# Kernel optimization log

Hardware: AMD Instinct MI355X
Metric: run time of the kernel (lower is better)

The kernel has to match this reference:

```python
import jax, jax.numpy as jnp
import numpy as np

M, K, L, OUT = 16, 64, 6, 128
IN_CH = 2 + 1 + 1 + 1 + 4 * L  # 29
HID_IN = 128 * 2 + 4           # 260


def setup_inputs() -> dict:
    key = jax.random.key(0)
    ks = jax.random.split(key, 5)
    N = 2_000_000
    P = jax.random.normal(ks[0], (N, 2), jnp.float32) * 2.0
    def lin(k, i, o):
        return jax.random.normal(k, (i, o), jnp.float32) / np.float32(np.sqrt(i))
    return {
        'P': P,
        'W1': lin(ks[1], IN_CH, 64), 'b1': jnp.zeros((64,), jnp.float32),
        'W2': lin(ks[2], 64, 128),   'b2': jnp.zeros((128,), jnp.float32),
        'W3': lin(ks[3], HID_IN, 128), 'b3': jnp.zeros((128,), jnp.float32),
        'W4': lin(ks[4], 128, OUT),  'b4': jnp.zeros((OUT,), jnp.float32),
    }


def _fps(P, m):
    # furthest point sampling, seeded at index 0 (standard convention)
    N = P.shape[0]
    def step(carry, _):
        min_d, last_idx = carry
        last = P[last_idx]
        d = jnp.sum((P - last) ** 2, axis=-1)          # [N]
        min_d = jnp.minimum(min_d, d)
        nxt = jnp.argmax(min_d)
        return (min_d, nxt), last_idx
    init = (jnp.full((N,), jnp.finfo(jnp.float32).max, jnp.float32), jnp.int32(0))
    (_, _), idxs = jax.lax.scan(step, init, None, length=m)
    return idxs  # [m] int


def _gelu(x):
    return jax.nn.gelu(x, approximate=False)  # torch nn.GELU default = erf


def reference(P, W1, b1, W2, b2, W3, b3, W4, b4):
    c_idx = jax.lax.stop_gradient(_fps(P, M))
    C = P[c_idx]                                       # [M,2]
    # brute-force kNN: expanded squared distance avoids [M,N,2] intermediate
    Ps = jax.lax.stop_gradient(P)
    Cs = jax.lax.stop_gradient(C)
    d2 = (jnp.sum(Ps ** 2, -1)[None, :]
          - 2.0 * Cs @ Ps.T
          + jnp.sum(Cs ** 2, -1)[:, None])             # [M,N]
    _, nidx = jax.lax.top_k(-d2, K)                    # [M,K]
    patch = P[nidx]                                    # [M,K,2]
    delta = patch - C[:, None, :]                      # [M,K,2]
    r = jnp.linalg.norm(delta, axis=-1, keepdims=True) # [M,K,1]
    theta = jnp.arctan2(delta[..., 1:2], delta[..., 0:1])
    freqs = (2.0 ** jnp.arange(L)).astype(jnp.float32) # [L]
    ang = delta[..., None, :] * freqs[:, None]         # [M,K,L,2]
    ff = jnp.concatenate([jnp.sin(ang), jnp.cos(ang)], -1).reshape(M, K, 4 * L)
    per_pt = jnp.concatenate([delta, r, jnp.sin(theta), jnp.cos(theta), ff], -1)  # [M,K,29]
    h = _gelu(per_pt @ W1 + b1)
    h = _gelu(h @ W2 + b2)                             # [M,K,128]
    h_max = h.max(axis=1)
    h_mean = h.mean(axis=1)
    rr = r[..., 0]                                     # [M,K]
    stats = jnp.stack([rr.mean(1), rr.max(1), rr.min(1), rr.std(1, ddof=1)], -1)  # [M,4]
    z = jnp.concatenate([h_max, h_mean, stats], -1)    # [M,260]
    F = _gelu(z @ W3 + b3) @ W4 + b4                   # [M,OUT]
    return F, C
```

## Files before the change

kernel.cpp:

```cpp
#include <hip/hip_runtime.h>
#include <math.h>

#define MCENT 16
#define KNN   64
#define NBINS 512
#define RBINS 256
#define CAP   7936
#define SKEYS 1024
#define FPSB  1024
#define FPST  256
#define MLPT  1024

__device__ __forceinline__ float gelu_f(float x){
    return 0.5f * x * (1.0f + erff(x * 0.70710678118654752440f));
}

__device__ __forceinline__ void xcd_slice(int NP, int B, int bid, int tpb, int tid,
                                          int* q0, int* s1, int* step){
    int xcd = bid & 7, j = bid >> 3, Bx = B >> 3;
    long long np = NP;
    *q0   = (int)((np * xcd) >> 3) + j*tpb + tid;
    *s1   = (int)((np * (xcd+1)) >> 3);
    *step = Bx * tpb;
}

__global__ __launch_bounds__(FPST) void fps_step(
    const float* __restrict__ P, int N,
    float* __restrict__ min_d,
    unsigned long long* __restrict__ partials,
    int k,
    float* __restrict__ cxy,
    float* __restrict__ outC,
    unsigned int* __restrict__ ghist,
    unsigned int* __restrict__ cnt)
{
    const int lane = threadIdx.x & 63;
    const int wid  = threadIdx.x >> 6;
    __shared__ unsigned long long wred[FPST/64];
    __shared__ int s_cur;

    if (k == 0){
        int gi = blockIdx.x*FPST + threadIdx.x;
        if (gi < MCENT*NBINS) ghist[gi] = 0u;
        if (gi < MCENT) cnt[gi] = 0u;
    }

    int cur = 0;
    if (k > 0){
        unsigned long long pb = 0ULL;
        for (int i = threadIdx.x; i < FPSB; i += FPST){
            unsigned long long v = partials[(k-1)*FPSB + i];
            if (v > pb) pb = v;
        }
#pragma unroll
        for (int off = 32; off > 0; off >>= 1){
            unsigned long long o = __shfl_xor(pb, off, 64);
            if (o > pb) pb = o;
        }
        if (lane == 0) wred[wid] = pb;
        __syncthreads();
        if (threadIdx.x == 0){
            unsigned long long b = wred[0];
#pragma unroll
            for (int w = 1; w < FPST/64; ++w) if (wred[w] > b) b = wred[w];
            s_cur = (int)(0xFFFFFFFFu - (unsigned)(b & 0xFFFFFFFFu));
        }
        __syncthreads();
        cur = s_cur;
    }

    if (blockIdx.x == 0 && threadIdx.x == 0){
        float cx = P[2*cur], cy = P[2*cur+1];
        cxy[2*k] = cx; cxy[2*k+1] = cy;
        outC[2*k] = cx; outC[2*k+1] = cy;
    }

    const float cx = P[2*cur], cy = P[2*cur+1];
    unsigned long long bk = 0ULL;
    const int NP = N >> 1;
    int q0, s1, st;
    xcd_slice(NP, gridDim.x, blockIdx.x, FPST, threadIdx.x, &q0, &s1, &st);
    for (int q = q0; q < s1; q += st){
        float4 p = ((const float4*)P)[q];
        float dx0 = __fsub_rn(p.x, cx), dy0 = __fsub_rn(p.y, cy);
        float d0  = __fadd_rn(__fmul_rn(dx0,dx0), __fmul_rn(dy0,dy0));
        float dx1 = __fsub_rn(p.z, cx), dy1 = __fsub_rn(p.w, cy);
        float d1  = __fadd_rn(__fmul_rn(dx1,dx1), __fmul_rn(dy1,dy1));
        float mx, my;
        if (k == 0){
            mx = d0; my = d1;
            ((float2*)min_d)[q] = make_float2(mx, my);
        } else {
            float2 mo = ((const float2*)min_d)[q];
            mx = fminf(mo.x, d0); my = fminf(mo.y, d1);
            if (mx != mo.x || my != mo.y)
                ((float2*)min_d)[q] = make_float2(mx, my);
        }
        int g = 2*q;
        unsigned long long k0 =
            ((unsigned long long)__float_as_uint(mx) << 32)
            | (unsigned long long)(0xFFFFFFFFu - (unsigned)g);
        unsigned long long k1 =
            ((unsigned long long)__float_as_uint(my) << 32)
            | (unsigned long long)(0xFFFFFFFFu - (unsigned)(g+1));
        if (k0 > bk) bk = k0;
        if (k1 > bk) bk = k1;
    }
    if ((N & 1) && blockIdx.x == 0 && threadIdx.x == 0){
        int g = N-1;
        float dx = __fsub_rn(P[2*g], cx), dy = __fsub_rn(P[2*g+1], cy);
        float d  = __fadd_rn(__fmul_rn(dx,dx), __fmul_rn(dy,dy));
        float nm = (k == 0) ? d : fminf(min_d[g], d);
        min_d[g] = nm;
        unsigned long long kk =
            ((unsigned long long)__float_as_uint(nm) << 32)
            | (unsigned long long)(0xFFFFFFFFu - (unsigned)g);
        if (kk > bk) bk = kk;
    }
#pragma unroll
    for (int off = 32; off > 0; off >>= 1){
        unsigned long long o = __shfl_xor(bk, off, 64);
        if (o > bk) bk = o;
    }
    if (lane == 0) wred[wid] = bk;
    __syncthreads();
    if (threadIdx.x == 0){
        unsigned long long b = wred[0];
#pragma unroll
        for (int w = 1; w < FPST/64; ++w) if (wred[w] > b) b = wred[w];
        partials[k*FPSB + blockIdx.x] = b;
    }
}

__global__ __launch_bounds__(256) void hist_kernel(
    const float* __restrict__ P, int N,
    const unsigned long long* __restrict__ partials,
    float* __restrict__ cxy,
    float* __restrict__ outC,
    unsigned int* __restrict__ ghist,
    unsigned int* __restrict__ rhist)
{
    __shared__ unsigned int h[MCENT*NBINS];
    __shared__ float scx[MCENT], scy[MCENT], scs2[MCENT];
    __shared__ unsigned long long wred[4];
    __shared__ int s_cur;

    {
        unsigned long long pb = 0ULL;
        for (int i = threadIdx.x; i < FPSB; i += 256){
            unsigned long long v = partials[14*FPSB + i];
            if (v > pb) pb = v;
        }
#pragma unroll
        for (int off = 32; off > 0; off >>= 1){
            unsigned long long o = __shfl_xor(pb, off, 64);
            if (o > pb) pb = o;
        }
        if ((threadIdx.x & 63) == 0) wred[threadIdx.x >> 6] = pb;
        __syncthreads();
        if (threadIdx.x == 0){
            unsigned long long b = wred[0];
#pragma unroll
            for (int w = 1; w < 4; ++w) if (wred[w] > b) b = wred[w];
            s_cur = (int)(0xFFFFFFFFu - (unsigned)(b & 0xFFFFFFFFu));
        }
        __syncthreads();
    }
    const int cur15 = s_cur;
    const float c15x = P[2*cur15], c15y = P[2*cur15+1];
    if (blockIdx.x == 0 && threadIdx.x == 0){
        cxy[30] = c15x; cxy[31] = c15y;
        outC[30] = c15x; outC[31] = c15y;
    }

    {
        int gi = blockIdx.x*blockDim.x + threadIdx.x;
        if (gi < MCENT*RBINS) rhist[gi] = 0u;
    }
    for (int i = threadIdx.x; i < MCENT*NBINS; i += blockDim.x) h[i] = 0u;
    if (threadIdx.x < MCENT){
        float a, b;
        if (threadIdx.x == 15){ a = c15x; b = c15y; }
        else { a = cxy[2*threadIdx.x]; b = cxy[2*threadIdx.x+1]; }
        scx[threadIdx.x] = a; scy[threadIdx.x] = b;
        scs2[threadIdx.x] = __fadd_rn(__fmul_rn(a,a), __fmul_rn(b,b));
    }
    __syncthreads();
    const int T    = gridDim.x * blockDim.x;
    const int NP16 = (N >> 1) >> 4;
    for (int q = blockIdx.x*blockDim.x + threadIdx.x; q < NP16; q += T){
        float4 p = ((const float4*)P)[(size_t)q << 4];
        float ps20 = __fadd_rn(__fmul_rn(p.x,p.x), __fmul_rn(p.y,p.y));
        float ps21 = __fadd_rn(__fmul_rn(p.z,p.z), __fmul_rn(p.w,p.w));
#pragma unroll
        for (int m = 0; m < MCENT; ++m){
            float dot0 = __fadd_rn(__fmul_rn(scx[m],p.x), __fmul_rn(scy[m],p.y));
            float d20  = __fadd_rn(__fsub_rn(ps20, __fmul_rn(2.0f,dot0)), scs2[m]);
            atomicAdd(&h[m*NBINS + (__float_as_uint(fmaxf(d20,0.0f)) >> 22)], 1u);
            float dot1 = __fadd_rn(__fmul_rn(scx[m],p.z), __fmul_rn(scy[m],p.w));
            float d21  = __fadd_rn(__fsub_rn(ps21, __fmul_rn(2.0f,dot1)), scs2[m]);
            atomicAdd(&h[m*NBINS + (__float_as_uint(fmaxf(d21,0.0f)) >> 22)], 1u);
        }
    }
    __syncthreads();
    for (int i = threadIdx.x; i < MCENT*NBINS; i += blockDim.x){
        unsigned v = h[i];
        if (v) atomicAdd(&ghist[i], v);
    }
}

__device__ __forceinline__ void compute_ssc(const unsigned* gh, int tid, float* ssc){
    if (tid < MCENT){
        unsigned cum = 0; int B = NBINS-1;
        for (int b = 0; b < NBINS; ++b){
            cum += gh[tid*NBINS + b];
            if (cum >= KNN){ B = b; break; }
        }
        ssc[tid] = 255.0f / __uint_as_float((unsigned)(B+1) << 22);
    }
}

__global__ __launch_bounds__(256) void refine_kernel(
    const float* __restrict__ P, int N,
    const float* __restrict__ cxy,
    const unsigned int* __restrict__ ghist,
    unsigned int* __restrict__ rhist)
{
    __shared__ unsigned int gh[MCENT*NBINS];
    __shared__ unsigned int h[MCENT*RBINS];
    __shared__ float scx[MCENT], scy[MCENT], scs2[MCENT], ssc[MCENT];
    for (int i = threadIdx.x; i < MCENT*NBINS; i += 256) gh[i] = ghist[i];
    for (int i = threadIdx.x; i < MCENT*RBINS; i += 256) h[i] = 0u;
    if (threadIdx.x < MCENT){
        float a = cxy[2*threadIdx.x], b = cxy[2*threadIdx.x+1];
        scx[threadIdx.x]=a; scy[threadIdx.x]=b;
        scs2[threadIdx.x]=__fadd_rn(__fmul_rn(a,a),__fmul_rn(b,b));
    }
    __syncthreads();
    compute_ssc(gh, threadIdx.x, ssc);
    __syncthreads();
    const int NP = N >> 1;
    int q0, s1, st;
    xcd_slice(NP, gridDim.x, blockIdx.x, 256, threadIdx.x, &q0, &s1, &st);
    for (int q = q0; q < s1; q += st){
        float4 p = ((const float4*)P)[q];
        float ps20 = __fadd_rn(__fmul_rn(p.x,p.x), __fmul_rn(p.y,p.y));
        float ps21 = __fadd_rn(__fmul_rn(p.z,p.z), __fmul_rn(p.w,p.w));
#pragma unroll
        for (int m = 0; m < MCENT; ++m){
            float dot0 = __fadd_rn(__fmul_rn(scx[m],p.x), __fmul_rn(scy[m],p.y));
            float d20  = __fadd_rn(__fsub_rn(ps20, __fmul_rn(2.0f,dot0)), scs2[m]);
            int b0 = (int)(fmaxf(d20, 0.0f) * ssc[m]);
            if (b0 < RBINS) atomicAdd(&h[m*RBINS + b0], 1u);
            float dot1 = __fadd_rn(__fmul_rn(scx[m],p.z), __fmul_rn(scy[m],p.w));
            float d21  = __fadd_rn(__fsub_rn(ps21, __fmul_rn(2.0f,dot1)), scs2[m]);
            int b1 = (int)(fmaxf(d21, 0.0f) * ssc[m]);
            if (b1 < RBINS) atomicAdd(&h[m*RBINS + b1], 1u);
        }
    }
    if ((N & 1) && blockIdx.x == 0 && threadIdx.x == 0){
        int g = N-1;
        float x = P[2*g], y = P[2*g+1];
        float ps2 = __fadd_rn(__fmul_rn(x,x), __fmul_rn(y,y));
        for (int m = 0; m < MCENT; ++m){
            float dot = __fadd_rn(__fmul_rn(scx[m],x), __fmul_rn(scy[m],y));
            float d2  = __fadd_rn(__fsub_rn(ps2, __fmul_rn(2.0f,dot)), scs2[m]);
            int b = (int)(fmaxf(d2, 0.0f) * ssc[m]);
            if (b < RBINS) atomicAdd(&h[m*RBINS + b], 1u);
        }
    }
    __syncthreads();
    for (int i = threadIdx.x; i < MCENT*RBINS; i += blockDim.x){
        unsigned v = h[i];
        if (v) atomicAdd(&rhist[i], v);
    }
}

__global__ __launch_bounds__(256) void collect_kernel(
    const float* __restrict__ P, int N,
    const float* __restrict__ cxy,
    const unsigned int* __restrict__ ghist,
    const unsigned int* __restrict__ rhist,
    unsigned int* __restrict__ cnt,
    float* __restrict__ cd2,
    int* __restrict__ cidx)
{
    __shared__ unsigned int gh[MCENT*NBINS];
    __shared__ unsigned int rh[MCENT*RBINS];
    __shared__ float scx[MCENT], scy[MCENT], scs2[MCENT], ssc[MCENT];
    __shared__ int sB2[MCENT];
    for (int i = threadIdx.x; i < MCENT*NBINS; i += 256) gh[i] = ghist[i];
    for (int i = threadIdx.x; i < MCENT*RBINS; i += 256) rh[i] = rhist[i];
    if (threadIdx.x < MCENT){
        float a = cxy[2*threadIdx.x], b = cxy[2*threadIdx.x+1];
        scx[threadIdx.x]=a; scy[threadIdx.x]=b;
        scs2[threadIdx.x]=__fadd_rn(__fmul_rn(a,a),__fmul_rn(b,b));
    }
    __syncthreads();
    compute_ssc(gh, threadIdx.x, ssc);
    if (threadIdx.x < MCENT){
        unsigned cum = 0; int B = RBINS-1;
        for (int b = 0; b < RBINS; ++b){
            cum += rh[threadIdx.x*RBINS + b];
            if (cum >= KNN){ B = b; break; }
        }
        sB2[threadIdx.x] = B;
    }
    __syncthreads();
    const int NP = N >> 1;
    int q0, s1, st;
    xcd_slice(NP, gridDim.x, blockIdx.x, 256, threadIdx.x, &q0, &s1, &st);
    for (int q = q0; q < s1; q += st){
        float4 p = ((const float4*)P)[q];
        float ps20 = __fadd_rn(__fmul_rn(p.x,p.x), __fmul_rn(p.y,p.y));
        float ps21 = __fadd_rn(__fmul_rn(p.z,p.z), __fmul_rn(p.w,p.w));
        int g = 2*q;
#pragma unroll
        for (int m = 0; m < MCENT; ++m){
            float dot0 = __fadd_rn(__fmul_rn(scx[m],p.x), __fmul_rn(scy[m],p.y));
            float d20  = __fadd_rn(__fsub_rn(ps20, __fmul_rn(2.0f,dot0)), scs2[m]);
            if ((int)(fmaxf(d20,0.0f) * ssc[m]) <= sB2[m]){
                unsigned pos = atomicAdd(&cnt[m], 1u);
                if (pos < CAP){ cd2[m*CAP+pos]=d20; cidx[m*CAP+pos]=g; }
            }
            float dot1 = __fadd_rn(__fmul_rn(scx[m],p.z), __fmul_rn(scy[m],p.w));
            float d21  = __fadd_rn(__fsub_rn(ps21, __fmul_rn(2.0f,dot1)), scs2[m]);
            if ((int)(fmaxf(d21,0.0f) * ssc[m]) <= sB2[m]){
                unsigned pos = atomicAdd(&cnt[m], 1u);
                if (pos < CAP){ cd2[m*CAP+pos]=d21; cidx[m*CAP+pos]=g+1; }
            }
        }
    }
    if ((N & 1) && blockIdx.x == 0 && threadIdx.x == 0){
        int g = N-1;
        float x = P[2*g], y = P[2*g+1];
        float ps2 = __fadd_rn(__fmul_rn(x,x), __fmul_rn(y,y));
        for (int m = 0; m < MCENT; ++m){
            float dot = __fadd_rn(__fmul_rn(scx[m],x), __fmul_rn(scy[m],y));
            float d2  = __fadd_rn(__fsub_rn(ps2, __fmul_rn(2.0f,dot)), scs2[m]);
            if ((int)(fmaxf(d2,0.0f) * ssc[m]) <= sB2[m]){
                unsigned pos = atomicAdd(&cnt[m], 1u);
                if (pos < CAP){ cd2[m*CAP+pos]=d2; cidx[m*CAP+pos]=g; }
            }
        }
    }
}

__global__ __launch_bounds__(MLPT) void mlp_kernel(
    const float* __restrict__ P,
    const float* __restrict__ cxy,
    const unsigned int* __restrict__ cnt,
    const float* __restrict__ cd2,
    const int* __restrict__ cidx,
    const float* __restrict__ W1, const float* __restrict__ b1,
    const float* __restrict__ W2, const float* __restrict__ b2,
    const float* __restrict__ W3, const float* __restrict__ b3,
    const float* __restrict__ W4, const float* __restrict__ b4,
    float* __restrict__ outF)
{
    const int m = blockIdx.x;
    const int tid = threadIdx.x;
    __shared__ float feat[KNN][32];
    __shared__ float h1s[KNN][64];
    __shared__ float sW1[29*64];
    __shared__ float sW2[64*128];
    __shared__ float pmax[8][128], psum[8][128];
    __shared__ float z[260];
    __shared__ float part[8][128];
    __shared__ float zz[128];
    __shared__ unsigned long long kkeys[SKEYS];
    __shared__ int snbr[KNN];

    {
        const float4* s2 = (const float4*)W2;
        float4* d2 = (float4*)sW2;
        d2[tid]        = s2[tid];
        d2[tid + 1024] = s2[tid + 1024];
        if (tid < 464) ((float4*)sW1)[tid] = ((const float4*)W1)[tid];
    }

    unsigned c = cnt[m]; if (c > CAP) c = CAP;
    if (c <= SKEYS){
        if (tid < (int)c){
            unsigned u = __float_as_uint(cd2[m*CAP+tid]);
            u = (u & 0x80000000u) ? ~u : (u | 0x80000000u);
            kkeys[tid] = ((unsigned long long)u << 32)
                       | (unsigned long long)(unsigned)cidx[m*CAP+tid];
        }
        __syncthreads();
        if (tid < (int)c){
            unsigned long long ki = kkeys[tid];
            int rank = 0;
            for (int j = 0; j < (int)c; ++j) rank += (kkeys[j] < ki);
            if (rank < KNN) snbr[rank] = (int)(unsigned)(ki & 0xFFFFFFFFu);
        }
    } else {
        for (int i = tid; i < (int)c; i += MLPT){
            unsigned ui = __float_as_uint(cd2[m*CAP+i]);
            ui = (ui & 0x80000000u) ? ~ui : (ui | 0x80000000u);
            unsigned long long ki = ((unsigned long long)ui << 32)
                                  | (unsigned long long)(unsigned)cidx[m*CAP+i];
            int rank = 0;
            for (int j = 0; j < (int)c; ++j){
                unsigned uj = __float_as_uint(cd2[m*CAP+j]);
                uj = (uj & 0x80000000u) ? ~uj : (uj | 0x80000000u);
                unsigned long long kj = ((unsigned long long)uj << 32)
                                      | (unsigned long long)(unsigned)cidx[m*CAP+j];
                rank += (kj < ki);
            }
            if (rank < KNN) snbr[rank] = (int)(unsigned)(ki & 0xFFFFFFFFu);
        }
    }
    __syncthreads();

    const float cx = cxy[2*m], cy = cxy[2*m+1];
    if (tid < KNN){
        int g = snbr[tid];
        float dx = P[2*g]   - cx;
        float dy = P[2*g+1] - cy;
        float r  = sqrtf(dx*dx + dy*dy);
        float th = atan2f(dy, dx);
        feat[tid][0]=dx; feat[tid][1]=dy; feat[tid][2]=r;
        feat[tid][3]=sinf(th); feat[tid][4]=cosf(th);
        float fx = dx, fy = dy;
#pragma unroll
        for (int l = 0; l < 6; ++l){
            feat[tid][5+4*l+0]=sinf(fx);
            feat[tid][5+4*l+1]=sinf(fy);
            feat[tid][5+4*l+2]=cosf(fx);
            feat[tid][5+4*l+3]=cosf(fy);
            fx += fx; fy += fy;
        }
    }
    __syncthreads();

#pragma unroll
    for (int rep = 0; rep < 4; ++rep){
        int o = rep*MLPT + tid;
        int k = o >> 6, j = o & 63;
        float acc = b1[j];
#pragma unroll
        for (int cc = 0; cc < 29; ++cc) acc += feat[k][cc] * sW1[cc*64 + j];
        h1s[k][j] = gelu_f(acc);
    }
    __syncthreads();

    {
        int j = tid & 127, kh = tid >> 7;
        float lmax = -3.402823466e+38f, lsum = 0.f;
        for (int kk = 0; kk < 8; ++kk){
            int k = kh*8 + kk;
            float acc = b2[j];
#pragma unroll 8
            for (int i = 0; i < 64; ++i) acc += h1s[k][i] * sW2[i*128 + j];
            float v = gelu_f(acc);
            lmax = fmaxf(lmax, v);
            lsum += v;
        }
        pmax[kh][j] = lmax; psum[kh][j] = lsum;
    }
    __syncthreads();
    if (tid < 128){
        float mx = pmax[0][tid], sm = psum[0][tid];
#pragma unroll
        for (int w = 1; w < 8; ++w){ mx = fmaxf(mx, pmax[w][tid]); sm += psum[w][tid]; }
        z[tid]       = mx;
        z[128 + tid] = sm * (1.0f/64.0f);
    }
    if (tid >= 128 && tid < 192){
        int l = tid - 128;
        float r = feat[l][2];
        float s = r, mx = r, mn = r;
        for (int off = 1; off < 64; off <<= 1){
            s  += __shfl_xor(s, off, 64);
            mx  = fmaxf(mx, __shfl_xor(mx, off, 64));
            mn  = fminf(mn, __shfl_xor(mn, off, 64));
        }
        float mean = s * (1.0f/64.0f);
        float dv = (r-mean)*(r-mean);
        for (int off = 1; off < 64; off <<= 1) dv += __shfl_xor(dv, off, 64);
        if (l == 0){
            z[256]=mean; z[257]=mx; z[258]=mn; z[259]=sqrtf(dv*(1.0f/63.0f));
        }
    }
    __syncthreads();

    {
        int j = tid & 127, seg = tid >> 7;
        int i0  = (seg < 4) ? seg*33 : 132 + (seg-4)*32;
        int cntn = (seg < 4) ? 33 : 32;
        float acc = 0.f;
        for (int i = i0; i < i0 + cntn; ++i) acc += z[i]*W3[i*128+j];
        part[seg][j] = acc;
    }
    __syncthreads();
    if (tid < 128){
        float a = part[0][tid];
#pragma unroll
        for (int w = 1; w < 8; ++w) a += part[w][tid];
        zz[tid] = gelu_f(a + b3[tid]);
    }
    __syncthreads();
    {
        int j = tid & 127, seg = tid >> 7;
        float acc = 0.f;
#pragma unroll
        for (int i = seg*16; i < seg*16+16; ++i) acc += zz[i]*W4[i*128+j];
        part[seg][j] = acc;
    }
    __syncthreads();
    if (tid < 128){
        float a = part[0][tid];
#pragma unroll
        for (int w = 1; w < 8; ++w) a += part[w][tid];
        outF[m*128 + tid] = a + b4[tid];
    }
}

extern "C" void kernel_launch(void* const* d_in, const int* in_sizes, int n_in,
                              void* d_out, int out_size, void* d_ws, size_t ws_size,
                              hipStream_t stream)
{
    const float* P  = (const float*)d_in[0];
    const float* W1 = (const float*)d_in[1];
    const float* b1 = (const float*)d_in[2];
    const float* W2 = (const float*)d_in[3];
    const float* b2 = (const float*)d_in[4];
    const float* W3 = (const float*)d_in[5];
    const float* b3 = (const float*)d_in[6];
    const float* W4 = (const float*)d_in[7];
    const float* b4 = (const float*)d_in[8];
    int N = in_sizes[0] / 2;
    float* outF = (float*)d_out;
    float* outC = outF + MCENT*128;
    (void)n_in; (void)out_size; (void)ws_size;

    char* base = (char*)d_ws;
    size_t off = 0;
    auto take = [&](size_t bytes)->char*{
        char* p = base + off;
        off = (off + bytes + 255) & ~(size_t)255;
        return p;
    };
    unsigned long long* partials = (unsigned long long*)take((size_t)MCENT*FPSB*8);
    float* cxy         = (float*)take(MCENT*2*4);
    unsigned int* ghist= (unsigned int*)take(MCENT*NBINS*4);
    unsigned int* rhist= (unsigned int*)take(MCENT*RBINS*4);
    unsigned int* cnt  = (unsigned int*)take(MCENT*4);
    float* cd2         = (float*)take((size_t)MCENT*CAP*4);
    int*   cidx        = (int*)  take((size_t)MCENT*CAP*4);
    float* min_d       = (float*)take((size_t)N*4);

    for (int k = 0; k < MCENT-1; ++k)
        fps_step<<<FPSB, FPST, 0, stream>>>(P, N, min_d, partials, k, cxy, outC,
                                            ghist, cnt);

    hist_kernel<<<128, 256, 0, stream>>>(P, N, partials, cxy, outC, ghist, rhist);
    refine_kernel<<<256, 256, 0, stream>>>(P, N, cxy, ghist, rhist);
    collect_kernel<<<512, 256, 0, stream>>>(P, N, cxy, ghist, rhist, cnt, cd2, cidx);
    mlp_kernel<<<MCENT, MLPT, 0, stream>>>(P, cxy, cnt, cd2, cidx,
                                           W1,b1,W2,b2,W3,b3,W4,b4, outF);
}
```

Before: 308.2 us.

## Fuse FPS iterations into one persistent cooperative kernel with register-resident points

Replaces the 15 per-iteration FPS kernel launches with a single cooperative kernel of 512x256 threads. Each thread keeps 16 points and their running min-distance in registers, and blocks synchronise across the grid through spin-waited atomic partials. This removes the per-step reloads of P and min_d from global memory and the launch overhead. The per-block histogram-threshold scans are moved into tiny separate kernels, and refine/collect now launch more blocks. The costs are spin-wait synchronisation, reliance on co-residency of all 512 blocks (enforced by the launch bounds of 2 blocks per CU), and extra small launches.

```diff
diff --git a/kernel.cpp b/kernel.cpp
--- a/kernel.cpp
+++ b/kernel.cpp
@@ -7,8 +7,9 @@
 #define RBINS 256
 #define CAP   7936
 #define SKEYS 1024
-#define FPSB  1024
+#define FPSB  512
 #define FPST  256
+#define NPT   16
 #define MLPT  1024
 
 __device__ __forceinline__ float gelu_f(float x){
@@ -24,32 +25,90 @@
     *step = Bx * tpb;
 }
 
-__global__ __launch_bounds__(FPST) void fps_step(
+__global__ void init_kernel(unsigned int* __restrict__ ghist,
+                            unsigned int* __restrict__ cnt,
+                            unsigned long long* __restrict__ partials){
+    const int T = gridDim.x * blockDim.x;
+    int t = blockIdx.x * blockDim.x + threadIdx.x;
+    for (int i = t; i < MCENT*NBINS; i += T) ghist[i] = 0u;
+    for (int i = t; i < (MCENT-1)*FPSB; i += T) partials[i] = 0ULL;
+    if (t < MCENT) cnt[t] = 0u;
+}
+
+__global__ __launch_bounds__(FPST, 2) void fps_coop(
     const float* __restrict__ P, int N,
-    float* __restrict__ min_d,
     unsigned long long* __restrict__ partials,
-    int k,
     float* __restrict__ cxy,
-    float* __restrict__ outC,
-    unsigned int* __restrict__ ghist,
-    unsigned int* __restrict__ cnt)
+    float* __restrict__ outC)
 {
+    const int T = FPSB * FPST;
+    const int t = blockIdx.x * FPST + threadIdx.x;
     const int lane = threadIdx.x & 63;
     const int wid  = threadIdx.x >> 6;
+
+    float px[NPT], py[NPT], md[NPT];
+#pragma unroll
+    for (int i = 0; i < NPT; ++i){
+        int g = t + i * T;
+        if (g < N){
+            float2 p = ((const float2*)P)[g];
+            px[i] = p.x; py[i] = p.y; md[i] = 3.402823466e+38f;
+        } else { px[i] = 0.f; py[i] = 0.f; md[i] = -1.0f; }
+    }
+
     __shared__ unsigned long long wred[FPST/64];
-    __shared__ int s_cur;
-
-    if (k == 0){
-        int gi = blockIdx.x*FPST + threadIdx.x;
-        if (gi < MCENT*NBINS) ghist[gi] = 0u;
-        if (gi < MCENT) cnt[gi] = 0u;
-    }
-
     int cur = 0;
-    if (k > 0){
+
+    for (int k = 0; k < MCENT; ++k){
+        if (blockIdx.x == 0 && threadIdx.x == 0){
+            float cx = P[2*cur], cy = P[2*cur+1];
+            cxy[2*k] = cx; cxy[2*k+1] = cy;
+            outC[2*k] = cx; outC[2*k+1] = cy;
+        }
+        if (k == MCENT-1) break;
+
+        const float cx = P[2*cur], cy = P[2*cur+1];
+        unsigned long long bk = 0ULL;
+#pragma unroll
+        for (int i = 0; i < NPT; ++i){
+            float dx = __fsub_rn(px[i], cx);
+            float dy = __fsub_rn(py[i], cy);
+            float d  = __fadd_rn(__fmul_rn(dx,dx), __fmul_rn(dy,dy));
+            if (md[i] >= 0.0f){
+                float nm = fminf(md[i], d);
+                md[i] = nm;
+                unsigned long long key =
+                    ((unsigned long long)__float_as_uint(nm) << 32)
+                    | (unsigned long long)(0xFFFFFFFFu - (unsigned)(t + i*T));
+                if (key > bk) bk = key;
+            }
+        }
+#pragma unroll
+        for (int off = 32; off > 0; off >>= 1){
+            unsigned long long o = __shfl_xor(bk, off, 64);
+            if (o > bk) bk = o;
+        }
+        if (lane == 0) wred[wid] = bk;
+        __syncthreads();
+        if (threadIdx.x == 0){
+            unsigned long long b = wred[0];
+#pragma unroll
+            for (int w = 1; w < FPST/64; ++w) if (wred[w] > b) b = wred[w];
+            __hip_atomic_store(&partials[k*FPSB + blockIdx.x], b,
+                               __ATOMIC_RELEASE, __HIP_MEMORY_SCOPE_AGENT);
+        }
+        __syncthreads();
+
         unsigned long long pb = 0ULL;
         for (int i = threadIdx.x; i < FPSB; i += FPST){
-            unsigned long long v = partials[(k-1)*FPSB + i];
+            const unsigned long long* slot = &partials[k*FPSB + i];
+            unsigned long long v = __hip_atomic_load(slot, __ATOMIC_RELAXED,
+                                                     __HIP_MEMORY_SCOPE_AGENT);
+            while (v == 0ULL){
+                __builtin_amdgcn_s_sleep(1);
+                v = __hip_atomic_load(slot, __ATOMIC_RELAXED,
+                                      __HIP_MEMORY_SCOPE_AGENT);
+            }
             if (v > pb) pb = v;
         }
 #pragma unroll
@@ -59,129 +118,29 @@
         }
         if (lane == 0) wred[wid] = pb;
         __syncthreads();
-        if (threadIdx.x == 0){
-            unsigned long long b = wred[0];
-#pragma unroll
-            for (int w = 1; w < FPST/64; ++w) if (wred[w] > b) b = wred[w];
-            s_cur = (int)(0xFFFFFFFFu - (unsigned)(b & 0xFFFFFFFFu));
-        }
+        unsigned long long fin = wred[0];
+#pragma unroll
+        for (int w = 1; w < FPST/64; ++w) if (wred[w] > fin) fin = wred[w];
         __syncthreads();
-        cur = s_cur;
-    }
-
-    if (blockIdx.x == 0 && threadIdx.x == 0){
-        float cx = P[2*cur], cy = P[2*cur+1];
-        cxy[2*k] = cx; cxy[2*k+1] = cy;
-        outC[2*k] = cx; outC[2*k+1] = cy;
-    }
-
-    const float cx = P[2*cur], cy = P[2*cur+1];
-    unsigned long long bk = 0ULL;
-    const int NP = N >> 1;
-    int q0, s1, st;
-    xcd_slice(NP, gridDim.x, blockIdx.x, FPST, threadIdx.x, &q0, &s1, &st);
-    for (int q = q0; q < s1; q += st){
-        float4 p = ((const float4*)P)[q];
-        float dx0 = __fsub_rn(p.x, cx), dy0 = __fsub_rn(p.y, cy);
-        float d0  = __fadd_rn(__fmul_rn(dx0,dx0), __fmul_rn(dy0,dy0));
-        float dx1 = __fsub_rn(p.z, cx), dy1 = __fsub_rn(p.w, cy);
-        float d1  = __fadd_rn(__fmul_rn(dx1,dx1), __fmul_rn(dy1,dy1));
-        float mx, my;
-        if (k == 0){
-            mx = d0; my = d1;
-            ((float2*)min_d)[q] = make_float2(mx, my);
-        } else {
-            float2 mo = ((const float2*)min_d)[q];
-            mx = fminf(mo.x, d0); my = fminf(mo.y, d1);
-            if (mx != mo.x || my != mo.y)
-                ((float2*)min_d)[q] = make_float2(mx, my);
-        }
-        int g = 2*q;
-        unsigned long long k0 =
-            ((unsigned long long)__float_as_uint(mx) << 32)
-            | (unsigned long long)(0xFFFFFFFFu - (unsigned)g);
-        unsigned long long k1 =
-            ((unsigned long long)__float_as_uint(my) << 32)
-            | (unsigned long long)(0xFFFFFFFFu - (unsigned)(g+1));
-        if (k0 > bk) bk = k0;
-        if (k1 > bk) bk = k1;
-    }
-    if ((N & 1) && blockIdx.x == 0 && threadIdx.x == 0){
-        int g = N-1;
-        float dx = __fsub_rn(P[2*g], cx), dy = __fsub_rn(P[2*g+1], cy);
-        float d  = __fadd_rn(__fmul_rn(dx,dx), __fmul_rn(dy,dy));
-        float nm = (k == 0) ? d : fminf(min_d[g], d);
-        min_d[g] = nm;
-        unsigned long long kk =
-            ((unsigned long long)__float_as_uint(nm) << 32)
-            | (unsigned long long)(0xFFFFFFFFu - (unsigned)g);
-        if (kk > bk) bk = kk;
-    }
-#pragma unroll
-    for (int off = 32; off > 0; off >>= 1){
-        unsigned long long o = __shfl_xor(bk, off, 64);
-        if (o > bk) bk = o;
-    }
-    if (lane == 0) wred[wid] = bk;
-    __syncthreads();
-    if (threadIdx.x == 0){
-        unsigned long long b = wred[0];
-#pragma unroll
-        for (int w = 1; w < FPST/64; ++w) if (wred[w] > b) b = wred[w];
-        partials[k*FPSB + blockIdx.x] = b;
+        cur = (int)(0xFFFFFFFFu - (unsigned)(fin & 0xFFFFFFFFu));
     }
 }
 
 __global__ __launch_bounds__(256) void hist_kernel(
     const float* __restrict__ P, int N,
-    const unsigned long long* __restrict__ partials,
-    float* __restrict__ cxy,
-    float* __restrict__ outC,
+    const float* __restrict__ cxy,
     unsigned int* __restrict__ ghist,
     unsigned int* __restrict__ rhist)
 {
     __shared__ unsigned int h[MCENT*NBINS];
     __shared__ float scx[MCENT], scy[MCENT], scs2[MCENT];
-    __shared__ unsigned long long wred[4];
-    __shared__ int s_cur;
-
-    {
-        unsigned long long pb = 0ULL;
-        for (int i = threadIdx.x; i < FPSB; i += 256){
-            unsigned long long v = partials[14*FPSB + i];
-            if (v > pb) pb = v;
-        }
-#pragma unroll
-        for (int off = 32; off > 0; off >>= 1){
-            unsigned long long o = __shfl_xor(pb, off, 64);
-            if (o > pb) pb = o;
-        }
-        if ((threadIdx.x & 63) == 0) wred[threadIdx.x >> 6] = pb;
-        __syncthreads();
-        if (threadIdx.x == 0){
-            unsigned long long b = wred[0];
-#pragma unroll
-            for (int w = 1; w < 4; ++w) if (wred[w] > b) b = wred[w];
-            s_cur = (int)(0xFFFFFFFFu - (unsigned)(b & 0xFFFFFFFFu));
-        }
-        __syncthreads();
-    }
-    const int cur15 = s_cur;
-    const float c15x = P[2*cur15], c15y = P[2*cur15+1];
-    if (blockIdx.x == 0 && threadIdx.x == 0){
-        cxy[30] = c15x; cxy[31] = c15y;
-        outC[30] = c15x; outC[31] = c15y;
-    }
-
     {
         int gi = blockIdx.x*blockDim.x + threadIdx.x;
         if (gi < MCENT*RBINS) rhist[gi] = 0u;
     }
     for (int i = threadIdx.x; i < MCENT*NBINS; i += blockDim.x) h[i] = 0u;
     if (threadIdx.x < MCENT){
-        float a, b;
-        if (threadIdx.x == 15){ a = c15x; b = c15y; }
-        else { a = cxy[2*threadIdx.x]; b = cxy[2*threadIdx.x+1]; }
+        float a = cxy[2*threadIdx.x], b = cxy[2*threadIdx.x+1];
         scx[threadIdx.x] = a; scy[threadIdx.x] = b;
         scs2[threadIdx.x] = __fadd_rn(__fmul_rn(a,a), __fmul_rn(b,b));
     }
@@ -209,35 +168,34 @@
     }
 }
 
-__device__ __forceinline__ void compute_ssc(const unsigned* gh, int tid, float* ssc){
-    if (tid < MCENT){
+__global__ void thr_kernel(const unsigned int* __restrict__ ghist,
+                           float* __restrict__ sc2){
+    int m = threadIdx.x;
+    if (m < MCENT){
         unsigned cum = 0; int B = NBINS-1;
         for (int b = 0; b < NBINS; ++b){
-            cum += gh[tid*NBINS + b];
+            cum += ghist[m*NBINS + b];
             if (cum >= KNN){ B = b; break; }
         }
-        ssc[tid] = 255.0f / __uint_as_float((unsigned)(B+1) << 22);
+        sc2[m] = 255.0f / __uint_as_float((unsigned)(B+1) << 22);
     }
 }
 
 __global__ __launch_bounds__(256) void refine_kernel(
     const float* __restrict__ P, int N,
     const float* __restrict__ cxy,
-    const unsigned int* __restrict__ ghist,
+    const float* __restrict__ sc2,
     unsigned int* __restrict__ rhist)
 {
-    __shared__ unsigned int gh[MCENT*NBINS];
     __shared__ unsigned int h[MCENT*RBINS];
     __shared__ float scx[MCENT], scy[MCENT], scs2[MCENT], ssc[MCENT];
-    for (int i = threadIdx.x; i < MCENT*NBINS; i += 256) gh[i] = ghist[i];
     for (int i = threadIdx.x; i < MCENT*RBINS; i += 256) h[i] = 0u;
     if (threadIdx.x < MCENT){
         float a = cxy[2*threadIdx.x], b = cxy[2*threadIdx.x+1];
         scx[threadIdx.x]=a; scy[threadIdx.x]=b;
         scs2[threadIdx.x]=__fadd_rn(__fmul_rn(a,a),__fmul_rn(b,b));
-    }
-    __syncthreads();
-    compute_ssc(gh, threadIdx.x, ssc);
+        ssc[threadIdx.x]=sc2[threadIdx.x];
+    }
     __syncthreads();
     const int NP = N >> 1;
     int q0, s1, st;
@@ -276,35 +234,36 @@
     }
 }
 
+__global__ void thr2_kernel(const unsigned int* __restrict__ rhist,
+                            int* __restrict__ B2){
+    int m = threadIdx.x;
+    if (m < MCENT){
+        unsigned cum = 0; int B = RBINS-1;
+        for (int b = 0; b < RBINS; ++b){
+            cum += rhist[m*RBINS + b];
+            if (cum >= KNN){ B = b; break; }
+        }
+        B2[m] = B;
+    }
+}
+
 __global__ __launch_bounds__(256) void collect_kernel(
     const float* __restrict__ P, int N,
     const float* __restrict__ cxy,
-    const unsigned int* __restrict__ ghist,
-    const unsigned int* __restrict__ rhist,
+    const float* __restrict__ sc2,
+    const int* __restrict__ B2,
     unsigned int* __restrict__ cnt,
     float* __restrict__ cd2,
     int* __restrict__ cidx)
 {
-    __shared__ unsigned int gh[MCENT*NBINS];
-    __shared__ unsigned int rh[MCENT*RBINS];
     __shared__ float scx[MCENT], scy[MCENT], scs2[MCENT], ssc[MCENT];
     __shared__ int sB2[MCENT];
-    for (int i = threadIdx.x; i < MCENT*NBINS; i += 256) gh[i] = ghist[i];
-    for (int i = threadIdx.x; i < MCENT*RBINS; i += 256) rh[i] = rhist[i];
     if (threadIdx.x < MCENT){
         float a = cxy[2*threadIdx.x], b = cxy[2*threadIdx.x+1];
         scx[threadIdx.x]=a; scy[threadIdx.x]=b;
         scs2[threadIdx.x]=__fadd_rn(__fmul_rn(a,a),__fmul_rn(b,b));
-    }
-    __syncthreads();
-    compute_ssc(gh, threadIdx.x, ssc);
-    if (threadIdx.x < MCENT){
-        unsigned cum = 0; int B = RBINS-1;
-        for (int b = 0; b < RBINS; ++b){
-            cum += rh[threadIdx.x*RBINS + b];
-            if (cum >= KNN){ B = b; break; }
-        }
-        sB2[threadIdx.x] = B;
+        ssc[threadIdx.x]=sc2[threadIdx.x];
+        sB2[threadIdx.x]=B2[threadIdx.x];
     }
     __syncthreads();
     const int NP = N >> 1;
@@ -542,22 +501,28 @@
         off = (off + bytes + 255) & ~(size_t)255;
         return p;
     };
-    unsigned long long* partials = (unsigned long long*)take((size_t)MCENT*FPSB*8);
+    unsigned long long* partials = (unsigned long long*)take((size_t)(MCENT-1)*FPSB*8);
     float* cxy         = (float*)take(MCENT*2*4);
     unsigned int* ghist= (unsigned int*)take(MCENT*NBINS*4);
     unsigned int* rhist= (unsigned int*)take(MCENT*RBINS*4);
     unsigned int* cnt  = (unsigned int*)take(MCENT*4);
+    float* sc2         = (float*)take(MCENT*4);
+    int*   B2          = (int*)  take(MCENT*4);
     float* cd2         = (float*)take((size_t)MCENT*CAP*4);
     int*   cidx        = (int*)  take((size_t)MCENT*CAP*4);
-    float* min_d       = (float*)take((size_t)N*4);
-
-    for (int k = 0; k < MCENT-1; ++k)
-        fps_step<<<FPSB, FPST, 0, stream>>>(P, N, min_d, partials, k, cxy, outC,
-                                            ghist, cnt);
-
-    hist_kernel<<<128, 256, 0, stream>>>(P, N, partials, cxy, outC, ghist, rhist);
-    refine_kernel<<<256, 256, 0, stream>>>(P, N, cxy, ghist, rhist);
-    collect_kernel<<<512, 256, 0, stream>>>(P, N, cxy, ghist, rhist, cnt, cd2, cidx);
+
+    init_kernel<<<32, 256, 0, stream>>>(ghist, cnt, partials);
+
+    void* fargs[] = { (void*)&P, (void*)&N, (void*)&partials,
+                      (void*)&cxy, (void*)&outC };
+    hipLaunchCooperativeKernel((const void*)fps_coop, dim3(FPSB), dim3(FPST),
+                               fargs, 0, stream);
+
+    hist_kernel<<<128, 256, 0, stream>>>(P, N, cxy, ghist, rhist);
+    thr_kernel<<<1, 64, 0, stream>>>(ghist, sc2);
+    refine_kernel<<<1024, 256, 0, stream>>>(P, N, cxy, sc2, rhist);
+    thr2_kernel<<<1, 64, 0, stream>>>(rhist, B2);
+    collect_kernel<<<1024, 256, 0, stream>>>(P, N, cxy, sc2, B2, cnt, cd2, cidx);
     mlp_kernel<<<MCENT, MLPT, 0, stream>>>(P, cxy, cnt, cd2, cidx,
                                            W1,b1,W2,b2,W3,b3,W4,b4, outF);
 }
```

New measurement: 379.0 us. +23.0%, slower.
